# Kernel optimization log

Measured on AMD Instinct MI355X. Metric: run time of the kernel, lower is better.

## Reference

```python
import jax, jax.numpy as jnp
import numpy as np

BS, DEG, H = 32, 4, 32
OUT = H  # n_aggr=1 inside Full -> out_size = n_aggr * h_size = h_size


def setup_inputs() -> dict:
    key = jax.random.key(0)
    k1, k2 = jax.random.split(key)
    neighbour_h = jax.random.normal(k1, (BS, DEG, H), dtype=jnp.float32)
    hp1 = H + 1
    t_shape = (hp1,) * DEG + (OUT,)  # [33,33,33,33,32]
    # xavier_uniform-like scale: fan_in = hp1**DEG, fan_out = OUT
    scale = float(np.sqrt(2.0 / (hp1 ** DEG + OUT)))
    T = jax.random.normal(k2, t_shape, dtype=jnp.float32) * scale
    return {"neighbour_h": neighbour_h, "T": T}


def reference(neighbour_h, T):
    # Full.forward: chunk neighbour_h along child dim, feed to AugmentedTensor.
    # AugmentedTensor: sequentially contract T against each child's augmented
    # embedding [h_i ; 1] over the leading axes of T.
    bs, deg, h = neighbour_h.shape
    hp1 = h + 1
    # augment with trailing 1 (bias slot): [bs, deg, h+1]
    h_aug = jnp.concatenate(
        [neighbour_h, jnp.ones((bs, deg, 1), neighbour_h.dtype)], axis=2
    )
    # first contraction: [bs, hp1] @ [hp1, hp1^(deg-1)*out]
    res = jnp.matmul(h_aug[:, 0, :], T.reshape(hp1, -1))
    # remaining contractions shrink the trailing dim by hp1 each step
    for i in range(1, deg):
        res = jnp.einsum("bi,bio->bo", h_aug[:, i, :], res.reshape(bs, hp1, -1))
    return res  # [bs, out_size] == [bs, h_size] since n_aggr=1
```

## Files before the change

### kernel.cpp

```cpp
#include <hip/hip_runtime.h>
#include <hip/hip_bf16.h>

#define HSZ 32
#define HP1 33
#define M3 35937
#define TI_STRIDE 1149984
#define NBLK 2247
#define RED_BLOCKS 64

typedef short bf16x8 __attribute__((ext_vector_type(8)));
typedef float f32x16 __attribute__((ext_vector_type(16)));

__device__ inline short f2bf(float f) {
  __hip_bfloat16 h = __float2bfloat16(f);
  return __builtin_bit_cast(short, h);
}

__global__ __launch_bounds__(64) void k_main(const float* __restrict__ T,
                                             const float* __restrict__ nh,
                                             float* __restrict__ tiles,
                                             float* __restrict__ out) {
  __shared__ float a0s[HP1 * 32];
  const int l = (int)threadIdx.x;
  const int bo = l & 31;
  const int g = l >> 5;
  const int m0 = (int)blockIdx.x * 16;

  for (int x = l; x < HP1 * 32; x += 64) {
    const int i = x >> 5;
    const int b = x & 31;
    a0s[x] = (i < HSZ) ? nh[b * 128 + i] : 1.0f;
  }

  if (blockIdx.x == 0) {
    const float4 z = make_float4(0.f, 0.f, 0.f, 0.f);
    for (int x = l; x < 256; x += 64) ((float4*)out)[x] = z;
  }

  float df[8];
  int ioff[8];
#pragma unroll
  for (int e = 0; e < 8; ++e) {
    const int mm = m0 + 8 * g + e;
    const bool valid = mm < M3;
    const int mc = valid ? mm : (M3 - 1);
    const int j = mc / 1089;
    const int r = mc - j * 1089;
    const int kk = r / 33;
    const int ll = r - kk * 33;
    const float a1 = (j < HSZ) ? nh[(bo * 4 + 1) * HSZ + j] : 1.0f;
    const float a2 = (kk < HSZ) ? nh[(bo * 4 + 2) * HSZ + kk] : 1.0f;
    const float a3 = (ll < HSZ) ? nh[(bo * 4 + 3) * HSZ + ll] : 1.0f;
    df[e] = valid ? (a1 * a2 * a3) : 0.0f;
    ioff[e] = mc * 32 + bo;
  }
  __syncthreads();

#define LOADT(buf, av, row)                               \
  {                                                       \
    const float* Tp = T + (size_t)(row) * TI_STRIDE;      \
    _Pragma("unroll")                                     \
    for (int e = 0; e < 8; ++e) buf[e] = Tp[ioff[e]];     \
    av = a0s[(row) * 32 + bo];                            \
  }
#define COMP(buf, av)                                                      \
  {                                                                        \
    bf16x8 af, bfr;                                                        \
    _Pragma("unroll")                                                      \
    for (int e = 0; e < 8; ++e) {                                          \
      af[e] = f2bf((av) * df[e]);                                          \
      bfr[e] = f2bf(buf[e]);                                               \
    }                                                                      \
    acc = __builtin_amdgcn_mfma_f32_32x32x16_bf16(af, bfr, acc, 0, 0, 0);  \
  }

  f32x16 acc = {};
  float t0[8], t1[8], t2[8], t3[8];
  float a0v, a1v, a2v, a3v;
  LOADT(t0, a0v, 0);
  LOADT(t1, a1v, 1);
  LOADT(t2, a2v, 2);
  for (int i = 0; i < 28; i += 4) {
    LOADT(t3, a3v, i + 3);
    COMP(t0, a0v);
    LOADT(t0, a0v, i + 4);
    COMP(t1, a1v);
    LOADT(t1, a1v, i + 5);
    COMP(t2, a2v);
    LOADT(t2, a2v, i + 6);
    COMP(t3, a3v);
  }
  LOADT(t3, a3v, 31);
  COMP(t0, a0v);
  LOADT(t0, a0v, 32);
  COMP(t1, a1v);
  COMP(t2, a2v);
  COMP(t3, a3v);
  COMP(t0, a0v);
#undef LOADT
#undef COMP

  float* tp = tiles + (size_t)blockIdx.x * 1024;
#pragma unroll
  for (int r = 0; r < 16; ++r) {
    const int brow = (r & 3) + 8 * (r >> 2) + 4 * g;
    tp[brow * 32 + bo] = acc[r];
  }
}

__global__ __launch_bounds__(256) void k_red(const float* __restrict__ tiles,
                                             float* __restrict__ out) {
  const int q = (int)blockIdx.x;
  const int tid = (int)threadIdx.x;
  float4 s0 = make_float4(0.f, 0.f, 0.f, 0.f);
  float4 s1 = make_float4(0.f, 0.f, 0.f, 0.f);
  int t = q;
  for (; t + RED_BLOCKS < NBLK; t += 2 * RED_BLOCKS) {
    const float4 v0 = *(const float4*)(tiles + (size_t)t * 1024 + tid * 4);
    const float4 v1 =
        *(const float4*)(tiles + (size_t)(t + RED_BLOCKS) * 1024 + tid * 4);
    s0.x += v0.x; s0.y += v0.y; s0.z += v0.z; s0.w += v0.w;
    s1.x += v1.x; s1.y += v1.y; s1.z += v1.z; s1.w += v1.w;
  }
  if (t < NBLK) {
    const float4 v0 = *(const float4*)(tiles + (size_t)t * 1024 + tid * 4);
    s0.x += v0.x; s0.y += v0.y; s0.z += v0.z; s0.w += v0.w;
  }
  atomicAdd(&out[tid * 4 + 0], s0.x + s1.x);
  atomicAdd(&out[tid * 4 + 1], s0.y + s1.y);
  atomicAdd(&out[tid * 4 + 2], s0.z + s1.z);
  atomicAdd(&out[tid * 4 + 3], s0.w + s1.w);
}

extern "C" void kernel_launch(void* const* d_in, const int* in_sizes, int n_in,
                              void* d_out, int out_size, void* d_ws, size_t ws_size,
                              hipStream_t stream) {
  const float* nh = (const float*)d_in[0];
  const float* T  = (const float*)d_in[1];
  float* out = (float*)d_out;
  float* tiles = (float*)d_ws;

  k_main<<<NBLK, 64, 0, stream>>>(T, nh, tiles, out);
  k_red<<<RED_BLOCKS, 256, 0, stream>>>(tiles, out);
}
```

Before: 47.59 us.

## Split K-loop across two waves per block and reduce partials in LDS

Each block now runs two wavefronts, each handling half of the 33 leading-axis rows, and their accumulators are summed through shared memory before the tile is written. Tile loads are issued before the df computation so global latency overlaps that setup work. The reduction kernel switches to contiguous per-block ranges with fewer blocks. The aim is more memory-level parallelism per CU on the T stream, at the cost of extra LDS traffic and a second barrier.

Measured after the change: 51.77 us. 8.8% more time.

```diff
diff --git a/kernel.cpp b/kernel.cpp
--- a/kernel.cpp
+++ b/kernel.cpp
@@ -6,7 +6,8 @@
 #define M3 35937
 #define TI_STRIDE 1149984
 #define NBLK 2247
-#define RED_BLOCKS 64
+#define RED_BLOCKS 32
+#define RED_PER 71
 
 typedef short bf16x8 __attribute__((ext_vector_type(8)));
 typedef float f32x16 __attribute__((ext_vector_type(16)));
@@ -16,17 +17,21 @@
   return __builtin_bit_cast(short, h);
 }
 
-__global__ __launch_bounds__(64) void k_main(const float* __restrict__ T,
-                                             const float* __restrict__ nh,
-                                             float* __restrict__ tiles,
-                                             float* __restrict__ out) {
+__global__ __launch_bounds__(128) void k_main(const float* __restrict__ T,
+                                              const float* __restrict__ nh,
+                                              float* __restrict__ tiles,
+                                              float* __restrict__ out) {
   __shared__ float a0s[HP1 * 32];
-  const int l = (int)threadIdx.x;
+  __shared__ float red[2][1024];
+  const int tid = (int)threadIdx.x;
+  const int w = tid >> 6;
+  const int l = tid & 63;
   const int bo = l & 31;
   const int g = l >> 5;
   const int m0 = (int)blockIdx.x * 16;
+  const int iBeg = w ? 16 : 0;
 
-  for (int x = l; x < HP1 * 32; x += 64) {
+  for (int x = tid; x < HP1 * 32; x += 128) {
     const int i = x >> 5;
     const int b = x & 31;
     a0s[x] = (i < HSZ) ? nh[b * 128 + i] : 1.0f;
@@ -34,34 +39,24 @@
 
   if (blockIdx.x == 0) {
     const float4 z = make_float4(0.f, 0.f, 0.f, 0.f);
-    for (int x = l; x < 256; x += 64) ((float4*)out)[x] = z;
+    for (int x = tid; x < 256; x += 128) ((float4*)out)[x] = z;
   }
 
-  float df[8];
   int ioff[8];
+  int mcv[8];
 #pragma unroll
   for (int e = 0; e < 8; ++e) {
     const int mm = m0 + 8 * g + e;
-    const bool valid = mm < M3;
-    const int mc = valid ? mm : (M3 - 1);
-    const int j = mc / 1089;
-    const int r = mc - j * 1089;
-    const int kk = r / 33;
-    const int ll = r - kk * 33;
-    const float a1 = (j < HSZ) ? nh[(bo * 4 + 1) * HSZ + j] : 1.0f;
-    const float a2 = (kk < HSZ) ? nh[(bo * 4 + 2) * HSZ + kk] : 1.0f;
-    const float a3 = (ll < HSZ) ? nh[(bo * 4 + 3) * HSZ + ll] : 1.0f;
-    df[e] = valid ? (a1 * a2 * a3) : 0.0f;
+    const int mc = (mm < M3) ? mm : (M3 - 1);
+    mcv[e] = (mm < M3) ? mm : -1;
     ioff[e] = mc * 32 + bo;
   }
-  __syncthreads();
 
-#define LOADT(buf, av, row)                               \
-  {                                                       \
-    const float* Tp = T + (size_t)(row) * TI_STRIDE;      \
-    _Pragma("unroll")                                     \
-    for (int e = 0; e < 8; ++e) buf[e] = Tp[ioff[e]];     \
-    av = a0s[(row) * 32 + bo];                            \
+#define LOADT(buf, row)                               \
+  {                                                   \
+    const float* Tp = T + (size_t)(row) * TI_STRIDE;  \
+    _Pragma("unroll")                                 \
+    for (int e = 0; e < 8; ++e) buf[e] = Tp[ioff[e]]; \
   }
 #define COMP(buf, av)                                                      \
   {                                                                        \
@@ -74,55 +69,99 @@
     acc = __builtin_amdgcn_mfma_f32_32x32x16_bf16(af, bfr, acc, 0, 0, 0);  \
   }
 
+  float t0[8], t1[8], t2[8], t3[8];
+  LOADT(t0, iBeg + 0);
+  LOADT(t1, iBeg + 1);
+  LOADT(t2, iBeg + 2);
+
+  float df[8];
+#pragma unroll
+  for (int e = 0; e < 8; ++e) {
+    const int mc = (mcv[e] >= 0) ? mcv[e] : (M3 - 1);
+    const int j = mc / 1089;
+    const int r = mc - j * 1089;
+    const int kk = r / 33;
+    const int ll = r - kk * 33;
+    const float a1 = (j < HSZ) ? nh[(bo * 4 + 1) * HSZ + j] : 1.0f;
+    const float a2 = (kk < HSZ) ? nh[(bo * 4 + 2) * HSZ + kk] : 1.0f;
+    const float a3 = (ll < HSZ) ? nh[(bo * 4 + 3) * HSZ + ll] : 1.0f;
+    df[e] = (mcv[e] >= 0) ? (a1 * a2 * a3) : 0.0f;
+  }
+  __syncthreads();
+
   f32x16 acc = {};
-  float t0[8], t1[8], t2[8], t3[8];
-  float a0v, a1v, a2v, a3v;
-  LOADT(t0, a0v, 0);
-  LOADT(t1, a1v, 1);
-  LOADT(t2, a2v, 2);
-  for (int i = 0; i < 28; i += 4) {
-    LOADT(t3, a3v, i + 3);
-    COMP(t0, a0v);
-    LOADT(t0, a0v, i + 4);
-    COMP(t1, a1v);
-    LOADT(t1, a1v, i + 5);
-    COMP(t2, a2v);
-    LOADT(t2, a2v, i + 6);
-    COMP(t3, a3v);
+  float av0 = a0s[(iBeg + 0) * 32 + bo];
+  float av1 = a0s[(iBeg + 1) * 32 + bo];
+  float av2 = a0s[(iBeg + 2) * 32 + bo];
+  float av3;
+
+  for (int ii = 0; ii < 3; ++ii) {
+    const int i = iBeg + 4 * ii;
+    LOADT(t3, i + 3);
+    av3 = a0s[(i + 3) * 32 + bo];
+    COMP(t0, av0);
+    LOADT(t0, i + 4);
+    av0 = a0s[(i + 4) * 32 + bo];
+    COMP(t1, av1);
+    LOADT(t1, i + 5);
+    av1 = a0s[(i + 5) * 32 + bo];
+    COMP(t2, av2);
+    LOADT(t2, i + 6);
+    av2 = a0s[(i + 6) * 32 + bo];
+    COMP(t3, av3);
   }
-  LOADT(t3, a3v, 31);
-  COMP(t0, a0v);
-  LOADT(t0, a0v, 32);
-  COMP(t1, a1v);
-  COMP(t2, a2v);
-  COMP(t3, a3v);
-  COMP(t0, a0v);
+  if (w == 0) {
+    LOADT(t3, 15);
+    av3 = a0s[15 * 32 + bo];
+    COMP(t0, av0);
+    COMP(t1, av1);
+    COMP(t2, av2);
+    COMP(t3, av3);
+  } else {
+    LOADT(t3, 31);
+    av3 = a0s[31 * 32 + bo];
+    COMP(t0, av0);
+    LOADT(t0, 32);
+    av0 = a0s[32 * 32 + bo];
+    COMP(t1, av1);
+    COMP(t2, av2);
+    COMP(t3, av3);
+    COMP(t0, av0);
+  }
 #undef LOADT
 #undef COMP
 
-  float* tp = tiles + (size_t)blockIdx.x * 1024;
 #pragma unroll
   for (int r = 0; r < 16; ++r) {
     const int brow = (r & 3) + 8 * (r >> 2) + 4 * g;
-    tp[brow * 32 + bo] = acc[r];
+    red[w][brow * 32 + bo] = acc[r];
   }
+  __syncthreads();
+  float* tp = tiles + (size_t)blockIdx.x * 1024 + tid * 8;
+  const float4 p0 = *(const float4*)&red[0][tid * 8];
+  const float4 p1 = *(const float4*)&red[1][tid * 8];
+  const float4 q0 = *(const float4*)&red[0][tid * 8 + 4];
+  const float4 q1 = *(const float4*)&red[1][tid * 8 + 4];
+  *(float4*)(tp)     = make_float4(p0.x + p1.x, p0.y + p1.y, p0.z + p1.z, p0.w + p1.w);
+  *(float4*)(tp + 4) = make_float4(q0.x + q1.x, q0.y + q1.y, q0.z + q1.z, q0.w + q1.w);
 }
 
 __global__ __launch_bounds__(256) void k_red(const float* __restrict__ tiles,
                                              float* __restrict__ out) {
   const int q = (int)blockIdx.x;
   const int tid = (int)threadIdx.x;
+  const int tBeg = q * RED_PER;
+  const int tEnd = (tBeg + RED_PER < NBLK) ? (tBeg + RED_PER) : NBLK;
   float4 s0 = make_float4(0.f, 0.f, 0.f, 0.f);
   float4 s1 = make_float4(0.f, 0.f, 0.f, 0.f);
-  int t = q;
-  for (; t + RED_BLOCKS < NBLK; t += 2 * RED_BLOCKS) {
+  int t = tBeg;
+  for (; t + 1 < tEnd; t += 2) {
     const float4 v0 = *(const float4*)(tiles + (size_t)t * 1024 + tid * 4);
-    const float4 v1 =
-        *(const float4*)(tiles + (size_t)(t + RED_BLOCKS) * 1024 + tid * 4);
+    const float4 v1 = *(const float4*)(tiles + (size_t)(t + 1) * 1024 + tid * 4);
     s0.x += v0.x; s0.y += v0.y; s0.z += v0.z; s0.w += v0.w;
     s1.x += v1.x; s1.y += v1.y; s1.z += v1.z; s1.w += v1.w;
   }
-  if (t < NBLK) {
+  if (t < tEnd) {
     const float4 v0 = *(const float4*)(tiles + (size_t)t * 1024 + tid * 4);
     s0.x += v0.x; s0.y += v0.y; s0.z += v0.z; s0.w += v0.w;
   }
@@ -140,6 +179,6 @@
   float* out = (float*)d_out;
   float* tiles = (float*)d_ws;
 
-  k_main<<<NBLK, 64, 0, stream>>>(T, nh, tiles, out);
+  k_main<<<NBLK, 128, 0, stream>>>(T, nh, tiles, out);
   k_red<<<RED_BLOCKS, 256, 0, stream>>>(tiles, out);
 }
```

## Precompute D outer-product, split reduction dim across two blocks per chunk

Applied to the files above, without the earlier changes.

A new pre-kernel materialises the per-batch product a1*a2*a3 vector D and the transposed a0 table in workspace, so k_main loads them instead of recomputing divisions and gathers per block. Each column chunk is now processed by two blocks, each covering half of the 33 leading rows, doubling the grid for more parallelism on a memory-bound stream of T. The reduction kernel is switched to contiguous ranges over the doubled tile count. This adds an extra launch and extra workspace traffic for D (about 4.6MB) and twice as many partial tiles to reduce.

Result: slower. 53.14 us (+11.7%).

```diff
diff --git a/kernel.cpp b/kernel.cpp
--- a/kernel.cpp
+++ b/kernel.cpp
@@ -4,9 +4,16 @@
 #define HSZ 32
 #define HP1 33
 #define M3 35937
+#define M3P 35952
 #define TI_STRIDE 1149984
-#define NBLK 2247
+#define NCHUNK 2247
+#define NBLK (2 * NCHUNK)
 #define RED_BLOCKS 64
+#define RED_PER 71
+
+#define OFF_A0T   0
+#define OFF_D     2048
+#define OFF_TILES 1154048
 
 typedef short bf16x8 __attribute__((ext_vector_type(8)));
 typedef float f32x16 __attribute__((ext_vector_type(16)));
@@ -16,52 +23,66 @@
   return __builtin_bit_cast(short, h);
 }
 
+__global__ __launch_bounds__(256) void k_pre(const float* __restrict__ nh,
+                                             float* __restrict__ a0T,
+                                             float* __restrict__ D,
+                                             float* __restrict__ out) {
+  const int b = blockIdx.y;
+  const int m = blockIdx.x * 256 + threadIdx.x;
+  if (m < M3P) {
+    float v = 0.f;
+    if (m < M3) {
+      const int j = m / 1089;
+      const int r = m - j * 1089;
+      const int k = r / 33;
+      const int l = r - k * 33;
+      const float a1 = (j < HSZ) ? nh[(b * 4 + 1) * HSZ + j] : 1.0f;
+      const float a2 = (k < HSZ) ? nh[(b * 4 + 2) * HSZ + k] : 1.0f;
+      const float a3 = (l < HSZ) ? nh[(b * 4 + 3) * HSZ + l] : 1.0f;
+      v = a1 * a2 * a3;
+    }
+    D[(size_t)b * M3P + m] = v;
+  }
+  if (blockIdx.x == 0 && threadIdx.x < HP1) {
+    const int i = threadIdx.x;
+    a0T[i * 32 + b] = (i < HSZ) ? nh[b * 128 + i] : 1.0f;
+  }
+  if (blockIdx.x == 1 && b == 0) {
+    ((float4*)out)[threadIdx.x] = make_float4(0.f, 0.f, 0.f, 0.f);
+  }
+}
+
 __global__ __launch_bounds__(64) void k_main(const float* __restrict__ T,
-                                             const float* __restrict__ nh,
-                                             float* __restrict__ tiles,
-                                             float* __restrict__ out) {
-  __shared__ float a0s[HP1 * 32];
+                                             const float* __restrict__ a0T,
+                                             const float* __restrict__ D,
+                                             float* __restrict__ tiles) {
+  const int blk = (int)blockIdx.x;
+  const int h = (blk >= NCHUNK) ? 1 : 0;
+  const int c = blk - h * NCHUNK;
   const int l = (int)threadIdx.x;
   const int bo = l & 31;
   const int g = l >> 5;
-  const int m0 = (int)blockIdx.x * 16;
+  const int m0 = c * 16;
+  const int iB = h ? 16 : 0;
 
-  for (int x = l; x < HP1 * 32; x += 64) {
-    const int i = x >> 5;
-    const int b = x & 31;
-    a0s[x] = (i < HSZ) ? nh[b * 128 + i] : 1.0f;
-  }
-
-  if (blockIdx.x == 0) {
-    const float4 z = make_float4(0.f, 0.f, 0.f, 0.f);
-    for (int x = l; x < 256; x += 64) ((float4*)out)[x] = z;
-  }
-
+  const float* dp = D + (size_t)bo * M3P + m0 + 8 * g;
   float df[8];
+  *(float4*)(df)     = *(const float4*)(dp);
+  *(float4*)(df + 4) = *(const float4*)(dp + 4);
   int ioff[8];
 #pragma unroll
   for (int e = 0; e < 8; ++e) {
     const int mm = m0 + 8 * g + e;
-    const bool valid = mm < M3;
-    const int mc = valid ? mm : (M3 - 1);
-    const int j = mc / 1089;
-    const int r = mc - j * 1089;
-    const int kk = r / 33;
-    const int ll = r - kk * 33;
-    const float a1 = (j < HSZ) ? nh[(bo * 4 + 1) * HSZ + j] : 1.0f;
-    const float a2 = (kk < HSZ) ? nh[(bo * 4 + 2) * HSZ + kk] : 1.0f;
-    const float a3 = (ll < HSZ) ? nh[(bo * 4 + 3) * HSZ + ll] : 1.0f;
-    df[e] = valid ? (a1 * a2 * a3) : 0.0f;
+    const int mc = (mm < M3) ? mm : (M3 - 1);
     ioff[e] = mc * 32 + bo;
   }
-  __syncthreads();
 
 #define LOADT(buf, av, row)                               \
   {                                                       \
     const float* Tp = T + (size_t)(row) * TI_STRIDE;      \
     _Pragma("unroll")                                     \
     for (int e = 0; e < 8; ++e) buf[e] = Tp[ioff[e]];     \
-    av = a0s[(row) * 32 + bo];                            \
+    av = a0T[(row) * 32 + bo];                            \
   }
 #define COMP(buf, av)                                                      \
   {                                                                        \
@@ -75,32 +96,41 @@
   }
 
   f32x16 acc = {};
-  float t0[8], t1[8], t2[8], t3[8];
-  float a0v, a1v, a2v, a3v;
-  LOADT(t0, a0v, 0);
-  LOADT(t1, a1v, 1);
-  LOADT(t2, a2v, 2);
-  for (int i = 0; i < 28; i += 4) {
-    LOADT(t3, a3v, i + 3);
-    COMP(t0, a0v);
-    LOADT(t0, a0v, i + 4);
-    COMP(t1, a1v);
-    LOADT(t1, a1v, i + 5);
-    COMP(t2, a2v);
-    LOADT(t2, a2v, i + 6);
-    COMP(t3, a3v);
+  float t0[8], t1[8], t2[8];
+  float av0, av1, av2;
+  LOADT(t0, av0, iB + 0);
+  LOADT(t1, av1, iB + 1);
+#pragma unroll 1
+  for (int k3 = 0; k3 < 4; ++k3) {
+    const int i = iB + 3 * k3;
+    LOADT(t2, av2, i + 2);
+    COMP(t0, av0);
+    LOADT(t0, av0, i + 3);
+    COMP(t1, av1);
+    LOADT(t1, av1, i + 4);
+    COMP(t2, av2);
   }
-  LOADT(t3, a3v, 31);
-  COMP(t0, a0v);
-  LOADT(t0, a0v, 32);
-  COMP(t1, a1v);
-  COMP(t2, a2v);
-  COMP(t3, a3v);
-  COMP(t0, a0v);
+  if (h == 0) {
+    LOADT(t2, av2, 14);
+    COMP(t0, av0);
+    LOADT(t0, av0, 15);
+    COMP(t1, av1);
+    COMP(t2, av2);
+    COMP(t0, av0);
+  } else {
+    LOADT(t2, av2, 30);
+    COMP(t0, av0);
+    LOADT(t0, av0, 31);
+    COMP(t1, av1);
+    LOADT(t1, av1, 32);
+    COMP(t2, av2);
+    COMP(t0, av0);
+    COMP(t1, av1);
+  }
 #undef LOADT
 #undef COMP
 
-  float* tp = tiles + (size_t)blockIdx.x * 1024;
+  float* tp = tiles + (size_t)blk * 1024;
 #pragma unroll
   for (int r = 0; r < 16; ++r) {
     const int brow = (r & 3) + 8 * (r >> 2) + 4 * g;
@@ -112,17 +142,18 @@
                                              float* __restrict__ out) {
   const int q = (int)blockIdx.x;
   const int tid = (int)threadIdx.x;
+  const int tBeg = q * RED_PER;
+  const int tEnd = (tBeg + RED_PER < NBLK) ? (tBeg + RED_PER) : NBLK;
   float4 s0 = make_float4(0.f, 0.f, 0.f, 0.f);
   float4 s1 = make_float4(0.f, 0.f, 0.f, 0.f);
-  int t = q;
-  for (; t + RED_BLOCKS < NBLK; t += 2 * RED_BLOCKS) {
+  int t = tBeg;
+  for (; t + 1 < tEnd; t += 2) {
     const float4 v0 = *(const float4*)(tiles + (size_t)t * 1024 + tid * 4);
-    const float4 v1 =
-        *(const float4*)(tiles + (size_t)(t + RED_BLOCKS) * 1024 + tid * 4);
+    const float4 v1 = *(const float4*)(tiles + (size_t)(t + 1) * 1024 + tid * 4);
     s0.x += v0.x; s0.y += v0.y; s0.z += v0.z; s0.w += v0.w;
     s1.x += v1.x; s1.y += v1.y; s1.z += v1.z; s1.w += v1.w;
   }
-  if (t < NBLK) {
+  if (t < tEnd) {
     const float4 v0 = *(const float4*)(tiles + (size_t)t * 1024 + tid * 4);
     s0.x += v0.x; s0.y += v0.y; s0.z += v0.z; s0.w += v0.w;
   }
@@ -138,8 +169,12 @@
   const float* nh = (const float*)d_in[0];
   const float* T  = (const float*)d_in[1];
   float* out = (float*)d_out;
-  float* tiles = (float*)d_ws;
+  float* ws = (float*)d_ws;
+  float* a0T   = ws + OFF_A0T;
+  float* D     = ws + OFF_D;
+  float* tiles = ws + OFF_TILES;
 
-  k_main<<<NBLK, 64, 0, stream>>>(T, nh, tiles, out);
+  k_pre<<<dim3(141, 32), 256, 0, stream>>>(nh, a0T, D, out);
+  k_main<<<NBLK, 64, 0, stream>>>(T, a0T, D, tiles);
   k_red<<<RED_BLOCKS, 256, 0, stream>>>(tiles, out);
 }
```
